# Optimization experiments

Hardware: AMD Instinct MI355X
Metric: run time of the kernel (lower is better)

## Reference

```python
import jax, jax.numpy as jnp
import numpy as np

N = 100000      # nodes
E = 1600000     # edges (avg degree 16)
F_IN = 128      # num_features
H = 64          # hidden_dim
C = 7           # num_classes


def setup_inputs() -> dict:
    key = jax.random.key(0)
    ks = jax.random.split(key, 9)
    x = jax.random.normal(ks[0], (N, F_IN), dtype=jnp.float32)
    edge_index = jax.random.randint(ks[1], (2, E), 0, N, dtype=jnp.int32)
    s1 = 1.0 / np.sqrt(F_IN)
    s2 = 1.0 / np.sqrt(H)
    # SAGEConv1: lin_l applied to aggregated neighbors, lin_r to root
    W1l = jax.random.uniform(ks[2], (F_IN, H), jnp.float32, -s1, s1)
    W1r = jax.random.uniform(ks[3], (F_IN, H), jnp.float32, -s1, s1)
    b1 = jax.random.uniform(ks[4], (H,), jnp.float32, -s1, s1)
    # SAGEConv2
    W2l = jax.random.uniform(ks[5], (H, C), jnp.float32, -s2, s2)
    W2r = jax.random.uniform(ks[6], (H, C), jnp.float32, -s2, s2)
    b2 = jax.random.uniform(ks[7], (C,), jnp.float32, -s2, s2)
    return {"x": x, "edge_index": edge_index, "W1l": W1l, "W1r": W1r,
            "b1": b1, "W2l": W2l, "W2r": W2r, "b2": b2}


def _segment_mean(vals, idx, num_segments):
    # scatter-mean: sum messages per destination node, divide by in-degree
    sums = jax.ops.segment_sum(vals, idx, num_segments=num_segments)
    cnt = jax.ops.segment_sum(jnp.ones(idx.shape, vals.dtype), idx,
                              num_segments=num_segments)
    return sums / jnp.maximum(cnt, 1.0)[:, None]


def reference(x, edge_index, W1l, W1r, b1, W2l, W2r, b2):
    src, dst = edge_index[0], edge_index[1]
    # SAGEConv 1: mean of neighbor (src) features at each dst, plus root term
    agg1 = _segment_mean(x[src], dst, N)              # [N, F_IN]
    h = agg1 @ W1l + x @ W1r + b1                     # [N, H]
    h = jax.nn.relu(h)
    # dropout is inactive in eval mode (deterministic reference)
    # SAGEConv 2
    agg2 = _segment_mean(h[src], dst, N)              # [N, H]
    out = agg2 @ W2l + h @ W2r + b2                   # [N, C]
    return jax.nn.log_softmax(out, axis=1)
```

## Files before the change

kernel.cpp:

```cpp
#include <hip/hip_runtime.h>
#include <cstdint>
#include <cstddef>


#define CAP 64
#define BINSZ 128
#define CH 4096

typedef __attribute__((ext_vector_type(8))) short bf16x8v;
typedef __attribute__((ext_vector_type(4))) float f32x4v;

__device__ __forceinline__ float bf2f(unsigned short u) {
  return __uint_as_float(((unsigned int)u) << 16);
}
__device__ __forceinline__ unsigned short f2bf(float f) {
  unsigned int x = __float_as_uint(f);
  unsigned int r = (x + 0x7fffu + ((x >> 16) & 1u)) >> 16;
  return (unsigned short)r;
}

__global__ __launch_bounds__(256) void k_hist(const int* __restrict__ ei,
                                              int* __restrict__ hist,
                                              int E, int NB, int NCH) {
  __shared__ int lcnt[1024];
  const int c = blockIdx.x, t = threadIdx.x;
  for (int i = t; i < NB; i += 256) lcnt[i] = 0;
  __syncthreads();
  const int base = c * CH;
  const int end = min(base + CH, E);
  for (int e = base + t; e < end; e += 256) {
    int d = ei[E + e];
    atomicAdd(&lcnt[d >> 7], 1);
  }
  __syncthreads();
  for (int i = t; i < NB; i += 256) hist[(size_t)i * NCH + c] = lcnt[i];
}

__global__ __launch_bounds__(256) void k_scanA(int* __restrict__ hist,
                                               int* __restrict__ tot,
                                               int NB, int NCH) {
  const int lane = threadIdx.x & 63;
  const int bin = blockIdx.x * 4 + (threadIdx.x >> 6);
  if (bin >= NB) return;
  int* h = hist + (size_t)bin * NCH;
  int carry = 0;
  for (int base = 0; base < NCH; base += 64) {
    int i = base + lane;
    int v = (i < NCH) ? h[i] : 0;
    int incl = v;
    #pragma unroll
    for (int d = 1; d < 64; d <<= 1) {
      int t = __shfl_up(incl, d, 64);
      if (lane >= d) incl += t;
    }
    if (i < NCH) h[i] = carry + incl - v;
    carry += __shfl(incl, 63, 64);
  }
  if (lane == 0) tot[bin] = carry;
}

__global__ __launch_bounds__(64) void k_scanB(const int* __restrict__ tot,
                                              int* __restrict__ binbase, int NB) {
  const int lane = threadIdx.x;
  int carry = 0;
  for (int base = 0; base < NB; base += 64) {
    int i = base + lane;
    int v = (i < NB) ? tot[i] : 0;
    int incl = v;
    #pragma unroll
    for (int d = 1; d < 64; d <<= 1) {
      int t = __shfl_up(incl, d, 64);
      if (lane >= d) incl += t;
    }
    if (i < NB) binbase[i] = carry + incl - v;
    carry += __shfl(incl, 63, 64);
  }
  if (lane == 0) binbase[NB] = carry;
}

__global__ __launch_bounds__(256) void k_scat(const int* __restrict__ ei,
                                              const int* __restrict__ hist,
                                              const int* __restrict__ binbase,
                                              unsigned int* __restrict__ part,
                                              int E, int NB, int NCH) {
  __shared__ int lcur[1024];
  const int c = blockIdx.x, t = threadIdx.x;
  for (int i = t; i < NB; i += 256)
    lcur[i] = hist[(size_t)i * NCH + c] + binbase[i];
  __syncthreads();
  const int base = c * CH;
  const int end = min(base + CH, E);
  for (int e = base + t; e < end; e += 256) {
    int s = ei[e];
    int d = ei[E + e];
    int bin = d >> 7;
    int pos = atomicAdd(&lcur[bin], 1);
    part[pos] = (unsigned)s | ((unsigned)(d & 127) << 17);
  }
}

__global__ __launch_bounds__(256) void k_bucketB(const int* __restrict__ binbase,
                                                 const unsigned int* __restrict__ part,
                                                 int* __restrict__ cnt,
                                                 int* __restrict__ bucket) {
  __shared__ int lbkt[BINSZ * CAP];
  __shared__ int ldeg[BINSZ];
  const int b = blockIdx.x, t = threadIdx.x;
  if (t < BINSZ) ldeg[t] = 0;
  __syncthreads();
  const int e0 = binbase[b], e1 = binbase[b + 1];
  for (int i = e0 + t; i < e1; i += 256) {
    unsigned rec = part[i];
    int loc = rec >> 17;
    int p = atomicAdd(&ldeg[loc], 1);
    if (p < CAP) lbkt[loc * CAP + p] = (int)(rec & 0x1FFFFu);
  }
  __syncthreads();
  if (t < BINSZ) cnt[b * BINSZ + t] = ldeg[t];
  const int4* s4 = (const int4*)lbkt;
  int4* d4 = (int4*)(bucket + (size_t)b * BINSZ * CAP);
  #pragma unroll 2
  for (int i = t; i < BINSZ * CAP / 4; i += 256) d4[i] = s4[i];
}

__global__ __launch_bounds__(256) void k_wprep(const float* __restrict__ W1l,
                                               const float* __restrict__ W1r,
                                               unsigned short* __restrict__ wswz) {
  int idx = blockIdx.x * 256 + threadIdx.x;
  int j = idx & 7;
  int lane = (idx >> 3) & 63;
  int c = (idx >> 9) & 7;
  int t4 = idx >> 12;
  int kk = t4 * 32 + (lane >> 4) * 8 + j;
  int nn = c * 16 + (lane & 15);
  float v = (nn < 64) ? W1l[kk * 64 + nn] : W1r[kk * 64 + (nn - 64)];
  wswz[idx] = f2bf(v);
}

__global__ __launch_bounds__(256) void k_gemm1(
    const float* __restrict__ x,
    const unsigned short* __restrict__ wswz,
    const float* __restrict__ b1,
    unsigned short* __restrict__ xl,
    unsigned short* __restrict__ hroot,
    int Nn) {
  __shared__ unsigned short Bsw[16384];
  const int t = threadIdx.x;
  {
    const uint4* src = (const uint4*)wswz;
    uint4* dst = (uint4*)Bsw;
    #pragma unroll
    for (int i = 0; i < 8; ++i) dst[t + i * 256] = src[t + i * 256];
  }
  __syncthreads();

  const int lane = t & 63;
  const int wid = t >> 6;
  const int quad = lane >> 4;
  const int m = lane & 15;
  const int rowA = blockIdx.x * 64 + wid * 16 + m;
  const float* xrow = x + (size_t)min(rowA, Nn - 1) * 128;

  f32x4v acc[8];
  #pragma unroll
  for (int c = 0; c < 8; ++c) acc[c] = (f32x4v){0.f, 0.f, 0.f, 0.f};

  #pragma unroll
  for (int t4 = 0; t4 < 4; ++t4) {
    const int koff = t4 * 32 + quad * 8;
    float4 a0 = *(const float4*)(xrow + koff);
    float4 a1 = *(const float4*)(xrow + koff + 4);
    bf16x8v af;
    af[0] = (short)f2bf(a0.x); af[1] = (short)f2bf(a0.y);
    af[2] = (short)f2bf(a0.z); af[3] = (short)f2bf(a0.w);
    af[4] = (short)f2bf(a1.x); af[5] = (short)f2bf(a1.y);
    af[6] = (short)f2bf(a1.z); af[7] = (short)f2bf(a1.w);
    #pragma unroll
    for (int c = 0; c < 8; ++c) {
      const bf16x8v bf_ = *(const bf16x8v*)&Bsw[(((t4 * 8 + c) * 64 + lane)) << 3];
      acc[c] = __builtin_amdgcn_mfma_f32_16x16x32_bf16(af, bf_, acc[c], 0, 0, 0);
    }
  }

  const int rbase = blockIdx.x * 64 + wid * 16 + quad * 4;
  #pragma unroll
  for (int c = 0; c < 8; ++c) {
    const int col = c * 16 + m;
    #pragma unroll
    for (int i = 0; i < 4; ++i) {
      const int r = rbase + i;
      if (r < Nn) {
        if (c < 4) xl[(size_t)r * 64 + col] = f2bf(acc[c][i]);
        else       hroot[(size_t)r * 64 + (col - 64)] = f2bf(acc[c][i] + b1[col - 64]);
      }
    }
  }
}

__global__ __launch_bounds__(256) void k_agg1(
    const int* __restrict__ cnt, const int* __restrict__ bucket,
    const unsigned int* __restrict__ xl32, const unsigned int* __restrict__ hroot32,
    unsigned int* __restrict__ hbuf32, int Nn) {
  const int lane = threadIdx.x & 63;
  const int q = lane & 15;
  const int g = lane >> 4;
  const int gw = blockIdx.x * (blockDim.x >> 6) + (threadIdx.x >> 6);
  const int nw = gridDim.x * (blockDim.x >> 6);
  for (int n = gw; n < Nn; n += nw) {
    int c = cnt[n];
    int m = c < CAP ? c : CAP;
    int sidx = (lane < m) ? bucket[(size_t)n * CAP + lane] : 0;
    if ((unsigned)sidx >= (unsigned)Nn) sidx = 0;
    uint2 hu = *(const uint2*)(hroot32 + (size_t)n * 32 + 2 * q);
    float a0 = 0.f, a1 = 0.f, a2 = 0.f, a3 = 0.f;
    int i = 0;
    for (; i + 16 <= m; i += 16) {
      int rA = __shfl(sidx, i + g, 64);
      int rB = __shfl(sidx, i + 4 + g, 64);
      int rC = __shfl(sidx, i + 8 + g, 64);
      int rD = __shfl(sidx, i + 12 + g, 64);
      uint2 uA = *(const uint2*)(xl32 + (size_t)rA * 32 + 2 * q);
      uint2 uB = *(const uint2*)(xl32 + (size_t)rB * 32 + 2 * q);
      uint2 uC = *(const uint2*)(xl32 + (size_t)rC * 32 + 2 * q);
      uint2 uD = *(const uint2*)(xl32 + (size_t)rD * 32 + 2 * q);
      a0 += (__uint_as_float(uA.x << 16) + __uint_as_float(uB.x << 16))
          + (__uint_as_float(uC.x << 16) + __uint_as_float(uD.x << 16));
      a1 += (__uint_as_float(uA.x & 0xFFFF0000u) + __uint_as_float(uB.x & 0xFFFF0000u))
          + (__uint_as_float(uC.x & 0xFFFF0000u) + __uint_as_float(uD.x & 0xFFFF0000u));
      a2 += (__uint_as_float(uA.y << 16) + __uint_as_float(uB.y << 16))
          + (__uint_as_float(uC.y << 16) + __uint_as_float(uD.y << 16));
      a3 += (__uint_as_float(uA.y & 0xFFFF0000u) + __uint_as_float(uB.y & 0xFFFF0000u))
          + (__uint_as_float(uC.y & 0xFFFF0000u) + __uint_as_float(uD.y & 0xFFFF0000u));
    }
    for (; i + 8 <= m; i += 8) {
      int rA = __shfl(sidx, i + g, 64);
      int rB = __shfl(sidx, i + 4 + g, 64);
      uint2 uA = *(const uint2*)(xl32 + (size_t)rA * 32 + 2 * q);
      uint2 uB = *(const uint2*)(xl32 + (size_t)rB * 32 + 2 * q);
      a0 += __uint_as_float(uA.x << 16) + __uint_as_float(uB.x << 16);
      a1 += __uint_as_float(uA.x & 0xFFFF0000u) + __uint_as_float(uB.x & 0xFFFF0000u);
      a2 += __uint_as_float(uA.y << 16) + __uint_as_float(uB.y << 16);
      a3 += __uint_as_float(uA.y & 0xFFFF0000u) + __uint_as_float(uB.y & 0xFFFF0000u);
    }
    for (; i < m; i += 4) {
      int e = i + g;
      int r = __shfl(sidx, e & 63, 64);
      uint2 u = *(const uint2*)(xl32 + (size_t)r * 32 + 2 * q);
      if (e < m) {
        a0 += __uint_as_float(u.x << 16);
        a1 += __uint_as_float(u.x & 0xFFFF0000u);
        a2 += __uint_as_float(u.y << 16);
        a3 += __uint_as_float(u.y & 0xFFFF0000u);
      }
    }
    a0 += __shfl_xor(a0, 16, 64); a0 += __shfl_xor(a0, 32, 64);
    a1 += __shfl_xor(a1, 16, 64); a1 += __shfl_xor(a1, 32, 64);
    a2 += __shfl_xor(a2, 16, 64); a2 += __shfl_xor(a2, 32, 64);
    a3 += __shfl_xor(a3, 16, 64); a3 += __shfl_xor(a3, 32, 64);
    if (g == 0) {
      float dd = c > 0 ? (float)c : 1.f;
      float h0 = fmaxf(a0 / dd + __uint_as_float(hu.x << 16), 0.f);
      float h1 = fmaxf(a1 / dd + __uint_as_float(hu.x & 0xFFFF0000u), 0.f);
      float h2 = fmaxf(a2 / dd + __uint_as_float(hu.y << 16), 0.f);
      float h3 = fmaxf(a3 / dd + __uint_as_float(hu.y & 0xFFFF0000u), 0.f);
      uint2 o;
      o.x = (unsigned)f2bf(h0) | ((unsigned)f2bf(h1) << 16);
      o.y = (unsigned)f2bf(h2) | ((unsigned)f2bf(h3) << 16);
      *(uint2*)(hbuf32 + (size_t)n * 32 + 2 * q) = o;
    }
  }
}

__global__ __launch_bounds__(128) void k_gemm2(
    const unsigned short* __restrict__ hbuf,
    const float* __restrict__ W2l, const float* __restrict__ W2r,
    const float* __restrict__ b2,
    float* __restrict__ hl, float* __restrict__ hr, int Nn) {
  __shared__ float tile[128 * 65];
  const int t = threadIdx.x;
  const int rowbase = blockIdx.x * 128;
  for (int idx = t; idx < 128 * 64; idx += 128) {
    int r = idx >> 6, k = idx & 63;
    int n = rowbase + r;
    tile[r * 65 + k] = (n < Nn) ? bf2f(hbuf[(size_t)n * 64 + k]) : 0.f;
  }
  __syncthreads();
  int n = rowbase + t;
  if (n >= Nn) return;
  float al[7] = {0, 0, 0, 0, 0, 0, 0};
  float ar[7] = {0, 0, 0, 0, 0, 0, 0};
  for (int k = 0; k < 64; ++k) {
    float hv = tile[t * 65 + k];
    #pragma unroll
    for (int c = 0; c < 7; ++c) {
      al[c] = fmaf(hv, W2l[k * 7 + c], al[c]);
      ar[c] = fmaf(hv, W2r[k * 7 + c], ar[c]);
    }
  }
  #pragma unroll
  for (int c = 0; c < 7; ++c) {
    hl[(size_t)n * 8 + c] = al[c];
    hr[(size_t)n * 8 + c] = ar[c] + b2[c];
  }
  hl[(size_t)n * 8 + 7] = 0.f;
  hr[(size_t)n * 8 + 7] = 0.f;
}

__global__ __launch_bounds__(256) void k_out(
    const int* __restrict__ cnt, const int* __restrict__ bucket,
    const float* __restrict__ hl, const float* __restrict__ hr,
    float* __restrict__ out, int Nn) {
  const int lane = threadIdx.x & 63;
  const int c = lane & 7;
  const int sub = lane >> 3;
  const int gw = blockIdx.x * (blockDim.x >> 6) + (threadIdx.x >> 6);
  const int n = gw * 8 + sub;
  if (n >= Nn) return;
  int cn = cnt[n];
  int m = cn < CAP ? cn : CAP;
  const bool act = (c < 7);
  float acc = 0.f;
  for (int e0 = 0; e0 < m; e0 += 8) {
    int bv = (e0 + c < m) ? bucket[(size_t)n * CAP + e0 + c] : 0;
    #pragma unroll
    for (int cc = 0; cc < 8; ++cc) {
      if (e0 + cc < m) {
        int s = __shfl(bv, (lane & 56) + cc, 64);
        if ((unsigned)s >= (unsigned)Nn) s = 0;
        if (act) acc += hl[(size_t)s * 8 + c];
      }
    }
  }
  float dd = cn > 0 ? (float)cn : 1.f;
  float v = act ? (acc / dd + hr[(size_t)n * 8 + c]) : -INFINITY;
  float mx = v;
  mx = fmaxf(mx, __shfl_xor(mx, 1, 8));
  mx = fmaxf(mx, __shfl_xor(mx, 2, 8));
  mx = fmaxf(mx, __shfl_xor(mx, 4, 8));
  float ex = act ? expf(v - mx) : 0.f;
  float s2 = ex;
  s2 += __shfl_xor(s2, 1, 8);
  s2 += __shfl_xor(s2, 2, 8);
  s2 += __shfl_xor(s2, 4, 8);
  float res = v - mx - logf(s2);
  if (act) out[(size_t)n * 7 + c] = res;
}

static inline size_t alignup(size_t v) { return (v + 255) & ~(size_t)255; }

extern "C" void kernel_launch(void* const* d_in, const int* in_sizes, int n_in,
                              void* d_out, int out_size, void* d_ws, size_t ws_size,
                              hipStream_t stream) {
  const int N = in_sizes[0] / 128;
  const int E = in_sizes[1] / 2;
  const int NB = (N + BINSZ - 1) / BINSZ;
  const int Np = NB * BINSZ;
  const int NCH = (E + CH - 1) / CH;

  const float* x   = (const float*)d_in[0];
  const int*   ei  = (const int*)d_in[1];
  const float* W1l = (const float*)d_in[2];
  const float* W1r = (const float*)d_in[3];
  const float* b1  = (const float*)d_in[4];
  const float* W2l = (const float*)d_in[5];
  const float* W2r = (const float*)d_in[6];
  const float* b2  = (const float*)d_in[7];
  float* out = (float*)d_out;

  char* p = (char*)d_ws;
  int* hist    = (int*)p;            p += alignup((size_t)NB * NCH * 4);
  int* tot     = (int*)p;            p += alignup((size_t)NB * 4);
  int* binbase = (int*)p;            p += alignup((size_t)(NB + 1) * 4);
  unsigned int* part = (unsigned int*)p; p += alignup((size_t)E * 4);
  int* cnt    = (int*)p;             p += alignup((size_t)Np * 4);
  int* bucket = (int*)p;             p += alignup((size_t)Np * CAP * 4);
  unsigned short* wswz = (unsigned short*)p; p += alignup((size_t)16384 * 2);
  unsigned short* xl    = (unsigned short*)p; p += alignup((size_t)N * 64 * 2);
  unsigned short* hroot = (unsigned short*)p; p += alignup((size_t)N * 64 * 2);
  unsigned short* hbuf  = (unsigned short*)p; p += alignup((size_t)N * 64 * 2);
  float* hl  = (float*)p;            p += alignup((size_t)N * 8 * 4);
  float* hr  = (float*)p;            p += alignup((size_t)N * 8 * 4);

  dim3 b256(256);
  k_hist<<<dim3(NCH), b256, 0, stream>>>(ei, hist, E, NB, NCH);
  k_scanA<<<dim3((NB + 3) / 4), b256, 0, stream>>>(hist, tot, NB, NCH);
  k_scanB<<<dim3(1), dim3(64), 0, stream>>>(tot, binbase, NB);
  k_scat<<<dim3(NCH), b256, 0, stream>>>(ei, hist, binbase, part, E, NB, NCH);
  k_bucketB<<<dim3(NB), b256, 0, stream>>>(binbase, part, cnt, bucket);
  k_wprep<<<dim3(64), b256, 0, stream>>>(W1l, W1r, wswz);
  k_gemm1<<<dim3((N + 63) / 64), b256, 0, stream>>>(x, wswz, b1, xl, hroot, N);
  k_agg1<<<dim3(2048), b256, 0, stream>>>(cnt, bucket,
      (const unsigned int*)xl, (const unsigned int*)hroot, (unsigned int*)hbuf, N);
  k_gemm2<<<dim3((N + 127) / 128), dim3(128), 0, stream>>>(hbuf, W2l, W2r, b2, hl, hr, N);
  const int waves_out = (N + 7) / 8;
  k_out<<<dim3((waves_out + 3) / 4), b256, 0, stream>>>(cnt, bucket, hl, hr, out, N);
}
```

Before: 252.6 us.

## Fuse bucket construction into layer-1 aggregation kernel using shared-memory buckets

Merges the per-bin bucket-building kernel with the first neighbor aggregation, so each block builds its 128-node adjacency buckets in LDS and then aggregates those nodes directly from shared memory instead of re-reading cnt/bucket from global. This removes one launch and the global reread of bucket lists for layer 1. Buckets are still written to global for the second layer. The trade-off is lower occupancy from 32KB LDS per block and a fixed grid of one block per bin, each wave serially handling 32 nodes, which may reduce latency hiding for the gathers.

```diff
diff --git a/kernel.cpp b/kernel.cpp
--- a/kernel.cpp
+++ b/kernel.cpp
@@ -99,30 +99,6 @@
   }
 }
 
-__global__ __launch_bounds__(256) void k_bucketB(const int* __restrict__ binbase,
-                                                 const unsigned int* __restrict__ part,
-                                                 int* __restrict__ cnt,
-                                                 int* __restrict__ bucket) {
-  __shared__ int lbkt[BINSZ * CAP];
-  __shared__ int ldeg[BINSZ];
-  const int b = blockIdx.x, t = threadIdx.x;
-  if (t < BINSZ) ldeg[t] = 0;
-  __syncthreads();
-  const int e0 = binbase[b], e1 = binbase[b + 1];
-  for (int i = e0 + t; i < e1; i += 256) {
-    unsigned rec = part[i];
-    int loc = rec >> 17;
-    int p = atomicAdd(&ldeg[loc], 1);
-    if (p < CAP) lbkt[loc * CAP + p] = (int)(rec & 0x1FFFFu);
-  }
-  __syncthreads();
-  if (t < BINSZ) cnt[b * BINSZ + t] = ldeg[t];
-  const int4* s4 = (const int4*)lbkt;
-  int4* d4 = (int4*)(bucket + (size_t)b * BINSZ * CAP);
-  #pragma unroll 2
-  for (int i = t; i < BINSZ * CAP / 4; i += 256) d4[i] = s4[i];
-}
-
 __global__ __launch_bounds__(256) void k_wprep(const float* __restrict__ W1l,
                                                const float* __restrict__ W1r,
                                                unsigned short* __restrict__ wswz) {
@@ -197,21 +173,45 @@
   }
 }
 
-__global__ __launch_bounds__(256) void k_agg1(
-    const int* __restrict__ cnt, const int* __restrict__ bucket,
+__global__ __launch_bounds__(256) void k_bagg(
+    const int* __restrict__ binbase, const unsigned int* __restrict__ part,
+    int* __restrict__ cnt, int* __restrict__ bucket,
     const unsigned int* __restrict__ xl32, const unsigned int* __restrict__ hroot32,
     unsigned int* __restrict__ hbuf32, int Nn) {
-  const int lane = threadIdx.x & 63;
+  __shared__ int lbkt[BINSZ * CAP];
+  __shared__ int ldeg[BINSZ];
+  const int b = blockIdx.x, t = threadIdx.x;
+  if (t < BINSZ) ldeg[t] = 0;
+  __syncthreads();
+  const int e0 = binbase[b], e1 = binbase[b + 1];
+  for (int i = e0 + t; i < e1; i += 256) {
+    unsigned rec = part[i];
+    int loc = rec >> 17;
+    int p = atomicAdd(&ldeg[loc], 1);
+    if (p < CAP) lbkt[loc * CAP + p] = (int)(rec & 0x1FFFFu);
+  }
+  __syncthreads();
+  if (t < BINSZ) cnt[b * BINSZ + t] = ldeg[t];
+  {
+    const int4* s4 = (const int4*)lbkt;
+    int4* d4 = (int4*)(bucket + (size_t)b * BINSZ * CAP);
+    #pragma unroll 2
+    for (int i = t; i < BINSZ * CAP / 4; i += 256) d4[i] = s4[i];
+  }
+
+  const int lane = t & 63;
+  const int wid = t >> 6;
   const int q = lane & 15;
   const int g = lane >> 4;
-  const int gw = blockIdx.x * (blockDim.x >> 6) + (threadIdx.x >> 6);
-  const int nw = gridDim.x * (blockDim.x >> 6);
-  for (int n = gw; n < Nn; n += nw) {
-    int c = cnt[n];
+  for (int j = 0; j < 32; ++j) {
+    const int r0 = wid * 32 + j;
+    const int node = b * BINSZ + r0;
+    if (node >= Nn) continue;
+    int c = ldeg[r0];
     int m = c < CAP ? c : CAP;
-    int sidx = (lane < m) ? bucket[(size_t)n * CAP + lane] : 0;
+    int sidx = (lane < m) ? lbkt[r0 * CAP + lane] : 0;
     if ((unsigned)sidx >= (unsigned)Nn) sidx = 0;
-    uint2 hu = *(const uint2*)(hroot32 + (size_t)n * 32 + 2 * q);
+    uint2 hu = *(const uint2*)(hroot32 + (size_t)node * 32 + 2 * q);
     float a0 = 0.f, a1 = 0.f, a2 = 0.f, a3 = 0.f;
     int i = 0;
     for (; i + 16 <= m; i += 16) {
@@ -266,7 +266,7 @@
       uint2 o;
       o.x = (unsigned)f2bf(h0) | ((unsigned)f2bf(h1) << 16);
       o.y = (unsigned)f2bf(h2) | ((unsigned)f2bf(h3) << 16);
-      *(uint2*)(hbuf32 + (size_t)n * 32 + 2 * q) = o;
+      *(uint2*)(hbuf32 + (size_t)node * 32 + 2 * q) = o;
     }
   }
 }
@@ -386,10 +386,9 @@
   k_scanA<<<dim3((NB + 3) / 4), b256, 0, stream>>>(hist, tot, NB, NCH);
   k_scanB<<<dim3(1), dim3(64), 0, stream>>>(tot, binbase, NB);
   k_scat<<<dim3(NCH), b256, 0, stream>>>(ei, hist, binbase, part, E, NB, NCH);
-  k_bucketB<<<dim3(NB), b256, 0, stream>>>(binbase, part, cnt, bucket);
   k_wprep<<<dim3(64), b256, 0, stream>>>(W1l, W1r, wswz);
   k_gemm1<<<dim3((N + 63) / 64), b256, 0, stream>>>(x, wswz, b1, xl, hroot, N);
-  k_agg1<<<dim3(2048), b256, 0, stream>>>(cnt, bucket,
+  k_bagg<<<dim3(NB), b256, 0, stream>>>(binbase, part, cnt, bucket,
       (const unsigned int*)xl, (const unsigned int*)hroot, (unsigned int*)hbuf, N);
   k_gemm2<<<dim3((N + 127) / 128), dim3(128), 0, stream>>>(hbuf, W2l, W2r, b2, hl, hr, N);
   const int waves_out = (N + 7) / 8;
```

Measured after the change: 275.2 us. +9.0%, slower.
